# Performance work log

Measured on AMD Instinct MI355X. Metric: run time of the kernel, lower is better.

Reference implementation:

```python
import jax, jax.numpy as jnp
import numpy as np

H = 128  # hidden_size
EPS = 1e-5


def _lstm_scan(pre, Whh, h0, c0):
    # pre: [L, B, 4H] = x @ Wih^T + bias, precomputed outside the scan
    def step(carry, g_in):
        h, c = carry
        gates = g_in + h @ Whh.T  # [B, 4H], PyTorch gate order i,f,g,o
        i, f, g, o = jnp.split(gates, 4, axis=-1)
        c = jax.nn.sigmoid(f) * c + jax.nn.sigmoid(i) * jnp.tanh(g)
        h = jax.nn.sigmoid(o) * jnp.tanh(c)
        return (h, c), h
    (_, _), hs = jax.lax.scan(step, (h0, c0), pre)
    return hs  # [L, B, H]


def setup_inputs() -> dict:
    key = jax.random.key(0)
    ks = jax.random.split(key, 12)
    B, L, D = 128, 512, 256
    s = 0.05
    inp = {
        "x": jax.random.normal(ks[0], (B, L, D), jnp.float32),
        "W_proj": jax.random.normal(ks[1], (D, D), jnp.float32) * s,
        "b_proj": jnp.zeros((D,), jnp.float32),
        "Wih_f": jax.random.normal(ks[2], (4 * H, D), jnp.float32) * s,
        "Whh_f": jax.random.normal(ks[3], (4 * H, H), jnp.float32) * s,
        "b_f": jnp.concatenate([jnp.zeros(H), jnp.ones(H), jnp.zeros(2 * H)]).astype(jnp.float32),
        "Wih_b": jax.random.normal(ks[4], (4 * H, D), jnp.float32) * s,
        "Whh_b": jax.random.normal(ks[5], (4 * H, H), jnp.float32) * s,
        "b_b": jnp.concatenate([jnp.zeros(H), jnp.ones(H), jnp.zeros(2 * H)]).astype(jnp.float32),
        "gamma": jnp.ones((2 * H,), jnp.float32),
        "beta": jnp.zeros((2 * H,), jnp.float32),
    }
    return inp


def reference(x, W_proj, b_proj, Wih_f, Whh_f, b_f, Wih_b, Whh_b, b_b, gamma, beta):
    B, L, D = x.shape
    # input projection
    xp = x @ W_proj.T + b_proj  # [B, L, D]
    xt = jnp.transpose(xp, (1, 0, 2))  # time-major [L, B, D]

    h0 = jnp.zeros((B, H), x.dtype)
    c0 = jnp.zeros((B, H), x.dtype)

    # precompute input contributions to gates (big batched GEMM)
    pre_f = jnp.einsum('lbd,gd->lbg', xt, Wih_f) + b_f  # [L, B, 4H]
    pre_b = jnp.einsum('lbd,gd->lbg', xt[::-1], Wih_b) + b_b

    hs_f = _lstm_scan(pre_f, Whh_f, h0, c0)           # [L, B, H]
    hs_b = _lstm_scan(pre_b, Whh_b, h0, c0)[::-1]     # reverse back to forward time

    out = jnp.concatenate([hs_f, hs_b], axis=-1)       # [L, B, 2H]
    out = jnp.transpose(out, (1, 0, 2))                # [B, L, 2H]

    # LayerNorm over last dim (eval mode; dropout is identity)
    mu = out.mean(axis=-1, keepdims=True)
    var = out.var(axis=-1, keepdims=True)
    out = (out - mu) * jax.lax.rsqrt(var + EPS) * gamma + beta
    return out
```

## Files before the change

kernel.cpp:

```cpp
#include <hip/hip_runtime.h>

#define NB 128
#define NL 512
#define ND 256
#define NG 1024

typedef __attribute__((ext_vector_type(8))) short bfv8;
typedef __attribute__((ext_vector_type(4))) float f32x4;

#define LOG2E 1.4426950408889634f
#define NSCALE (-1.4426950408889634f)
#define GSCALE (2.8853900817779268f)

__device__ __forceinline__ unsigned short f2bf(float f) {
    unsigned u = __float_as_uint(f);
    u += 0x7fffu + ((u >> 16) & 1u);
    return (unsigned short)(u >> 16);
}
__device__ __forceinline__ float bf2f(unsigned short u) {
    return __uint_as_float(((unsigned)u) << 16);
}

__global__ __launch_bounds__(256) void convert_kernel(const float* __restrict__ x,
                                                      unsigned short* __restrict__ xbt) {
    size_t t = (size_t)blockIdx.x * 256 + threadIdx.x;
    size_t e = t * 4;
    int d = (int)(e & 255u);
    int l = (int)((e >> 8) & 511u);
    int b = (int)(e >> 17);
    float4 v = *(const float4*)(x + e);
    ushort4 o;
    o.x = f2bf(v.x); o.y = f2bf(v.y); o.z = f2bf(v.z); o.w = f2bf(v.w);
    *(ushort4*)(xbt + ((size_t)(l * NB + b)) * ND + d) = o;
}

__global__ __launch_bounds__(256) void fold_kernel(const float* __restrict__ Wproj,
                                                   const float* __restrict__ bproj,
                                                   const float* __restrict__ Wih_f,
                                                   const float* __restrict__ b_f,
                                                   const float* __restrict__ Wih_b,
                                                   const float* __restrict__ b_b,
                                                   unsigned short* __restrict__ weff,
                                                   float* __restrict__ beff) {
    int g = blockIdx.x;
    int k = threadIdx.x;
    int dirg = g >> 9;
    int rem  = g & 511;
    int hidg = rem >> 2;
    int gate = rem & 3;
    int srcrow = gate * 128 + hidg;
    float scale = (gate == 2) ? GSCALE : NSCALE;
    const float* Wih = dirg ? (Wih_b + (size_t)srcrow * ND) : (Wih_f + (size_t)srcrow * ND);
    float acc = 0.f;
    for (int d = 0; d < ND; ++d)
        acc += Wih[d] * Wproj[(size_t)d * ND + k];
    weff[(size_t)g * ND + k] = f2bf(acc * scale);
    if (k == 0) {
        float ab = dirg ? b_b[srcrow] : b_f[srcrow];
        for (int d = 0; d < ND; ++d) ab += Wih[d] * bproj[d];
        beff[g] = ab * scale;
    }
}

__global__ __launch_bounds__(256, 2) void gemm_pre(const unsigned short* __restrict__ A,
                                                   const unsigned short* __restrict__ Bw,
                                                   const float* __restrict__ bias,
                                                   unsigned short* __restrict__ C) {
    __shared__ unsigned short As[128 * 32];
    __shared__ unsigned short Bs[128 * 32];
    const int tid = threadIdx.x;
    const int lane = tid & 63;
    const int wid = tid >> 6;
    const int m0 = blockIdx.y * 128;
    const int n0 = blockIdx.x * 128;
    const int wm = (wid >> 1) * 64;
    const int wn = (wid & 1) * 64;

    f32x4 acc[4][4] = {};

    const int row0 = tid >> 2;
    const int row1 = row0 + 64;
    const int co = (tid & 3) * 8;
    const int sw = (((tid & 3) << 4) ^ ((row0 & 3) << 4)) >> 1;

    bfv8 ra0 = *(const bfv8*)(A + (size_t)(m0 + row0) * ND + co);
    bfv8 ra1 = *(const bfv8*)(A + (size_t)(m0 + row1) * ND + co);
    bfv8 rb0 = *(const bfv8*)(Bw + (size_t)(n0 + row0) * ND + co);
    bfv8 rb1 = *(const bfv8*)(Bw + (size_t)(n0 + row1) * ND + co);

    for (int it = 0; it < 8; ++it) {
        __syncthreads();
        *(bfv8*)(As + row0 * 32 + sw) = ra0;
        *(bfv8*)(As + row1 * 32 + sw) = ra1;
        *(bfv8*)(Bs + row0 * 32 + sw) = rb0;
        *(bfv8*)(Bs + row1 * 32 + sw) = rb1;
        const int k1 = ((it + 1) & 7) * 32;
        ra0 = *(const bfv8*)(A + (size_t)(m0 + row0) * ND + k1 + co);
        ra1 = *(const bfv8*)(A + (size_t)(m0 + row1) * ND + k1 + co);
        rb0 = *(const bfv8*)(Bw + (size_t)(n0 + row0) * ND + k1 + co);
        rb1 = *(const bfv8*)(Bw + (size_t)(n0 + row1) * ND + k1 + co);
        __syncthreads();

        const int r = lane & 15;
        const int kq = lane >> 4;
        bfv8 af[4], bfr[4];
        #pragma unroll
        for (int m = 0; m < 4; ++m) {
            int rw = wm + m * 16 + r;
            af[m] = *(const bfv8*)(As + rw * 32 + (((kq << 4) ^ ((rw & 3) << 4)) >> 1));
        }
        #pragma unroll
        for (int n = 0; n < 4; ++n) {
            int rw = wn + n * 16 + r;
            bfr[n] = *(const bfv8*)(Bs + rw * 32 + (((kq << 4) ^ ((rw & 3) << 4)) >> 1));
        }
        #pragma unroll
        for (int m = 0; m < 4; ++m)
            #pragma unroll
            for (int n = 0; n < 4; ++n)
                acc[m][n] = __builtin_amdgcn_mfma_f32_16x16x32_bf16(af[m], bfr[n], acc[m][n], 0, 0, 0);
    }

    const int r = lane & 15;
    const int rq = lane >> 4;
    #pragma unroll
    for (int n = 0; n < 4; ++n) {
        int col = n0 + wn + n * 16 + r;
        float bv = bias[col];
        #pragma unroll
        for (int m = 0; m < 4; ++m) {
            #pragma unroll
            for (int v = 0; v < 4; ++v) {
                int rowg = m0 + wm + m * 16 + rq * 4 + v;
                C[(size_t)rowg * NG + col] = f2bf(acc[m][n][v] + bv);
            }
        }
    }
}

struct ScanSM {
    unsigned short h[2][136];
    char pin[81700];
};

#define MFMA16(a, b, c) __builtin_amdgcn_mfma_f32_16x16x32_bf16((a), (b), (c), 0, 0, 0)

#define STEP(S, CURB, NXTB)                                                    \
  {                                                                            \
    int rr = (S) + 2; if (rr > 511) rr = 511;                \
    int tts = dirs ? (511 - rr) : rr;                                          \
    const unsigned short* rowp = pdb + (size_t)tts * (NB * NG);                \
    uint2 nx = *(const uint2*)(rowp + hid4);                \
    bfv8 ha0 = *(const bfv8*)&sm.h[CURB][q * 8];                               \
    bfv8 ha1 = *(const bfv8*)&sm.h[CURB][32 + q * 8];                          \
    bfv8 ha2 = *(const bfv8*)&sm.h[CURB][64 + q * 8];                          \
    bfv8 ha3 = *(const bfv8*)&sm.h[CURB][96 + q * 8];                          \
    f32x4 z = {0.f, 0.f, 0.f, 0.f};                                            \
    f32x4 iA = MFMA16(ha0, bfr[0][0], z);                                      \
    f32x4 fA = MFMA16(ha0, bfr[1][0], z);                                      \
    f32x4 gA = MFMA16(ha0, bfr[2][0], z);                                      \
    f32x4 oA = MFMA16(ha0, bfr[3][0], z);                                      \
    f32x4 iB = MFMA16(ha2, bfr[0][2], z);                                      \
    f32x4 fB = MFMA16(ha2, bfr[1][2], z);                                      \
    f32x4 gB = MFMA16(ha2, bfr[2][2], z);                                      \
    f32x4 oB = MFMA16(ha2, bfr[3][2], z);                                      \
    iA = MFMA16(ha1, bfr[0][1], iA); fA = MFMA16(ha1, bfr[1][1], fA);          \
    gA = MFMA16(ha1, bfr[2][1], gA); oA = MFMA16(ha1, bfr[3][1], oA);          \
    iB = MFMA16(ha3, bfr[0][3], iB); fB = MFMA16(ha3, bfr[1][3], fB);          \
    gB = MFMA16(ha3, bfr[2][3], gB); oB = MFMA16(ha3, bfr[3][3], oB);          \
    int tt = dirs ? (511 - (S)) : (S);                                         \
    {                                                                          \
        float pi = __uint_as_float(pP0.x << 16);                               \
        float pf = __uint_as_float(pP0.x & 0xffff0000u);                       \
        float pg = __uint_as_float(pP0.y << 16);                               \
        float po = __uint_as_float(pP0.y & 0xffff0000u);                       \
                 \
        float ia = __builtin_amdgcn_rcpf(1.f + __builtin_amdgcn_exp2f(iA[0] + iB[0] + pi)); \
        float fa = __builtin_amdgcn_rcpf(1.f + __builtin_amdgcn_exp2f(fA[0] + fB[0] + pf)); \
        float rg = __builtin_amdgcn_rcpf(1.f + __builtin_amdgcn_exp2f(gA[0] + gB[0] + pg)); \
        float oa = __builtin_amdgcn_rcpf(1.f + __builtin_amdgcn_exp2f(oA[0] + oB[0] + po)); \
        float ga = fmaf(-2.f, rg, 1.f);                                        \
        c0 = fmaf(fa, c0, ia * ga);                                            \
        float rc = __builtin_amdgcn_rcpf(1.f + __builtin_amdgcn_exp2f(c0 * GSCALE)); \
        float th = fmaf(-2.f, rc, 1.f);                                        \
        unsigned short us = f2bf(oa * th);                                     \
        if (q == 0) {                                                          \
            sm.h[NXTB][hid] = us;                                              \
            hsrow[(size_t)tt * 256 + hid] = us;                                \
        }                                                                      \
    }                                                                          \
    pP0 = pP1; pP1 = nx;                                                       \
    __builtin_amdgcn_sched_barrier(0);                                         \
    asm volatile("s_waitcnt lgkmcnt(0)");                                      \
    __builtin_amdgcn_s_barrier();                                              \
    __builtin_amdgcn_sched_barrier(0);                                         \
  }

__global__ void __launch_bounds__(512)
scan_kernel(const unsigned short* __restrict__ pre,
            const float* __restrict__ Whh_f,
            const float* __restrict__ Whh_b,
            unsigned short* __restrict__ hs) {
    const int b    = blockIdx.x;
    const int dirs = blockIdx.y;
    const int tid  = threadIdx.x;
    const int w    = tid >> 6;
    const int lane = tid & 63;
    const int r    = lane & 15;
    const int q    = lane >> 4;
    const int hid  = 16 * w + r;
    const int hid4 = hid * 4;

    __shared__ ScanSM sm;

    const float* __restrict__ Wd = dirs ? Whh_b : Whh_f;
    bfv8 bfr[4][4];
    #pragma unroll
    for (int g = 0; g < 4; ++g) {
        const float wscale = (g == 2) ? GSCALE : NSCALE;
        #pragma unroll
        for (int kk = 0; kk < 4; ++kk) {
            const float* src = Wd + (size_t)(g * 128 + hid) * 128 + kk * 32 + q * 8;
            float4 lo = *(const float4*)(src);
            float4 hi = *(const float4*)(src + 4);
            bfv8 v;
            v[0] = (short)f2bf(lo.x * wscale); v[1] = (short)f2bf(lo.y * wscale);
            v[2] = (short)f2bf(lo.z * wscale); v[3] = (short)f2bf(lo.w * wscale);
            v[4] = (short)f2bf(hi.x * wscale); v[5] = (short)f2bf(hi.y * wscale);
            v[6] = (short)f2bf(hi.z * wscale); v[7] = (short)f2bf(hi.w * wscale);
            bfr[g][kk] = v;
        }
    }

    if (q == 0) sm.h[0][hid] = 0;

    float c0 = 0.f;

    const unsigned short* pdb = pre + (size_t)b * NG + dirs * 512;
    unsigned short* hsrow = hs + (size_t)b * NL * 256 + dirs * 128;

    int t0 = dirs ? 511 : 0;
    int t1 = dirs ? 510 : 1;
    uint2 pP0 = *(const uint2*)(pdb + (size_t)t0 * (NB * NG) + hid4);
    uint2 pP1 = *(const uint2*)(pdb + (size_t)t1 * (NB * NG) + hid4);
    __syncthreads();

    for (int s = 0; s < 512; s += 2) {
        STEP(s, 0, 1)
        STEP(s + 1, 1, 0)
    }
}

__global__ __launch_bounds__(256) void ln_kernel(const unsigned short* __restrict__ hs,
                                                 float* __restrict__ out,
                                                 const float* __restrict__ gamma,
                                                 const float* __restrict__ beta) {
    int row = blockIdx.x * 4 + (threadIdx.x >> 6);
    int lane = threadIdx.x & 63;
    const ushort4 hv = ((const ushort4*)(hs + (size_t)row * 256))[lane];
    float a = bf2f(hv.x), bb = bf2f(hv.y), c = bf2f(hv.z), d = bf2f(hv.w);
    float s = (a + bb) + (c + d);
    float s2 = (a * a + bb * bb) + (c * c + d * d);
    #pragma unroll
    for (int o = 32; o > 0; o >>= 1) {
        s += __shfl_xor(s, o);
        s2 += __shfl_xor(s2, o);
    }
    float mu = s * (1.f / 256.f);
    float var = s2 * (1.f / 256.f) - mu * mu;
    float rs = rsqrtf(var + 1e-5f);
    float4 gv = ((const float4*)gamma)[lane];
    float4 bv = ((const float4*)beta)[lane];
    float4 rr;
    rr.x = (a - mu) * rs * gv.x + bv.x;
    rr.y = (bb - mu) * rs * gv.y + bv.y;
    rr.z = (c - mu) * rs * gv.z + bv.z;
    rr.w = (d - mu) * rs * gv.w + bv.w;
    ((float4*)(out + (size_t)row * 256))[lane] = rr;
}

extern "C" void kernel_launch(void* const* d_in, const int* in_sizes, int n_in,
                              void* d_out, int out_size, void* d_ws, size_t ws_size,
                              hipStream_t stream) {
    (void)in_sizes; (void)n_in; (void)out_size; (void)ws_size;
    const float* x     = (const float*)d_in[0];
    const float* Wproj = (const float*)d_in[1];
    const float* bproj = (const float*)d_in[2];
    const float* Wih_f = (const float*)d_in[3];
    const float* Whh_f = (const float*)d_in[4];
    const float* b_f   = (const float*)d_in[5];
    const float* Wih_b = (const float*)d_in[6];
    const float* Whh_b = (const float*)d_in[7];
    const float* b_b   = (const float*)d_in[8];
    const float* gamma = (const float*)d_in[9];
    const float* beta  = (const float*)d_in[10];
    float* out = (float*)d_out;

    char* ws = (char*)d_ws;
    unsigned short* pre  = (unsigned short*)ws;
    unsigned short* xbt  = (unsigned short*)(ws + 134217728);
    unsigned short* hs   = xbt;
    unsigned short* weff = (unsigned short*)(ws + 167772160);
    float*          beff = (float*)(ws + 168296448);

    convert_kernel<<<16384, 256, 0, stream>>>(x, xbt);
    fold_kernel<<<1024, 256, 0, stream>>>(Wproj, bproj, Wih_f, b_f, Wih_b, b_b, weff, beff);
    gemm_pre<<<dim3(8, 512), 256, 0, stream>>>(xbt, weff, beff, pre);
    scan_kernel<<<dim3(128, 2), 512, 0, stream>>>(pre, Whh_f, Whh_b, hs);
    ln_kernel<<<16384, 256, 0, stream>>>(hs, out, gamma, beta);
}
```

Baseline: 363.2 us.

## Use direct global-to-LDS loads in GEMM and single accumulator chain in LSTM step

The input-projection GEMM now uses global_load_lds to copy tiles straight into shared memory, with a source-side swizzle, in place of register-staged loads. The register prefetch of the next tile is dropped, so loads are issued and waited on within the same iteration. The recurrent step now chains all four K-chunks into one accumulator per gate instead of two partial accumulators summed afterwards. This saves adds and registers but lengthens the serial MFMA dependency chain on the latency-critical scan.

```diff
diff --git a/kernel.cpp b/kernel.cpp
--- a/kernel.cpp
+++ b/kernel.cpp
@@ -7,6 +7,9 @@
 
 typedef __attribute__((ext_vector_type(8))) short bfv8;
 typedef __attribute__((ext_vector_type(4))) float f32x4;
+
+typedef __attribute__((address_space(1))) const unsigned int glo_u32;
+typedef __attribute__((address_space(3))) unsigned int lds_u32;
 
 #define LOG2E 1.4426950408889634f
 #define NSCALE (-1.4426950408889634f)
@@ -78,27 +81,24 @@
 
     f32x4 acc[4][4] = {};
 
-    const int row0 = tid >> 2;
-    const int row1 = row0 + 64;
-    const int co = (tid & 3) * 8;
-    const int sw = (((tid & 3) << 4) ^ ((row0 & 3) << 4)) >> 1;
-
-    bfv8 ra0 = *(const bfv8*)(A + (size_t)(m0 + row0) * ND + co);
-    bfv8 ra1 = *(const bfv8*)(A + (size_t)(m0 + row1) * ND + co);
-    bfv8 rb0 = *(const bfv8*)(Bw + (size_t)(n0 + row0) * ND + co);
-    bfv8 rb1 = *(const bfv8*)(Bw + (size_t)(n0 + row1) * ND + co);
+    const int srow = tid >> 2;
+    const int csrc = (lane & 3) ^ (srow & 3);
+    unsigned short* a_l0 = As + wid * 512;
+    unsigned short* a_l1 = As + 2048 + wid * 512;
+    unsigned short* b_l0 = Bs + wid * 512;
+    unsigned short* b_l1 = Bs + 2048 + wid * 512;
 
     for (int it = 0; it < 8; ++it) {
         __syncthreads();
-        *(bfv8*)(As + row0 * 32 + sw) = ra0;
-        *(bfv8*)(As + row1 * 32 + sw) = ra1;
-        *(bfv8*)(Bs + row0 * 32 + sw) = rb0;
-        *(bfv8*)(Bs + row1 * 32 + sw) = rb1;
-        const int k1 = ((it + 1) & 7) * 32;
-        ra0 = *(const bfv8*)(A + (size_t)(m0 + row0) * ND + k1 + co);
-        ra1 = *(const bfv8*)(A + (size_t)(m0 + row1) * ND + k1 + co);
-        rb0 = *(const bfv8*)(Bw + (size_t)(n0 + row0) * ND + k1 + co);
-        rb1 = *(const bfv8*)(Bw + (size_t)(n0 + row1) * ND + k1 + co);
+        const int kb = it * 32;
+        const unsigned short* ga0 = A  + (size_t)(m0 + srow) * ND + kb + csrc * 8;
+        const unsigned short* ga1 = A  + (size_t)(m0 + srow + 64) * ND + kb + csrc * 8;
+        const unsigned short* gb0 = Bw + (size_t)(n0 + srow) * ND + kb + csrc * 8;
+        const unsigned short* gb1 = Bw + (size_t)(n0 + srow + 64) * ND + kb + csrc * 8;
+        __builtin_amdgcn_global_load_lds((glo_u32*)ga0, (lds_u32*)a_l0, 16, 0, 0);
+        __builtin_amdgcn_global_load_lds((glo_u32*)ga1, (lds_u32*)a_l1, 16, 0, 0);
+        __builtin_amdgcn_global_load_lds((glo_u32*)gb0, (lds_u32*)b_l0, 16, 0, 0);
+        __builtin_amdgcn_global_load_lds((glo_u32*)gb1, (lds_u32*)b_l1, 16, 0, 0);
         __syncthreads();
 
         const int r = lane & 15;
@@ -107,12 +107,12 @@
         #pragma unroll
         for (int m = 0; m < 4; ++m) {
             int rw = wm + m * 16 + r;
-            af[m] = *(const bfv8*)(As + rw * 32 + (((kq << 4) ^ ((rw & 3) << 4)) >> 1));
+            af[m] = *(const bfv8*)(As + rw * 32 + ((((kq << 4) ^ ((rw & 3) << 4))) >> 1));
         }
         #pragma unroll
         for (int n = 0; n < 4; ++n) {
             int rw = wn + n * 16 + r;
-            bfr[n] = *(const bfv8*)(Bs + rw * 32 + (((kq << 4) ^ ((rw & 3) << 4)) >> 1));
+            bfr[n] = *(const bfv8*)(Bs + rw * 32 + ((((kq << 4) ^ ((rw & 3) << 4))) >> 1));
         }
         #pragma unroll
         for (int m = 0; m < 4; ++m)
@@ -156,18 +156,16 @@
     bfv8 ha2 = *(const bfv8*)&sm.h[CURB][64 + q * 8];                          \
     bfv8 ha3 = *(const bfv8*)&sm.h[CURB][96 + q * 8];                          \
     f32x4 z = {0.f, 0.f, 0.f, 0.f};                                            \
-    f32x4 iA = MFMA16(ha0, bfr[0][0], z);                                      \
-    f32x4 fA = MFMA16(ha0, bfr[1][0], z);                                      \
-    f32x4 gA = MFMA16(ha0, bfr[2][0], z);                                      \
-    f32x4 oA = MFMA16(ha0, bfr[3][0], z);                                      \
-    f32x4 iB = MFMA16(ha2, bfr[0][2], z);                                      \
-    f32x4 fB = MFMA16(ha2, bfr[1][2], z);                                      \
-    f32x4 gB = MFMA16(ha2, bfr[2][2], z);                                      \
-    f32x4 oB = MFMA16(ha2, bfr[3][2], z);                                      \
-    iA = MFMA16(ha1, bfr[0][1], iA); fA = MFMA16(ha1, bfr[1][1], fA);          \
-    gA = MFMA16(ha1, bfr[2][1], gA); oA = MFMA16(ha1, bfr[3][1], oA);          \
-    iB = MFMA16(ha3, bfr[0][3], iB); fB = MFMA16(ha3, bfr[1][3], fB);          \
-    gB = MFMA16(ha3, bfr[2][3], gB); oB = MFMA16(ha3, bfr[3][3], oB);          \
+    f32x4 acci = MFMA16(ha0, bfr[0][0], z);                                    \
+    f32x4 accf = MFMA16(ha0, bfr[1][0], z);                                    \
+    f32x4 accg = MFMA16(ha0, bfr[2][0], z);                                    \
+    f32x4 acco = MFMA16(ha0, bfr[3][0], z);                                    \
+    acci = MFMA16(ha1, bfr[0][1], acci); accf = MFMA16(ha1, bfr[1][1], accf);  \
+    accg = MFMA16(ha1, bfr[2][1], accg); acco = MFMA16(ha1, bfr[3][1], acco);  \
+    acci = MFMA16(ha2, bfr[0][2], acci); accf = MFMA16(ha2, bfr[1][2], accf);  \
+    accg = MFMA16(ha2, bfr[2][2], accg); acco = MFMA16(ha2, bfr[3][2], acco);  \
+    acci = MFMA16(ha3, bfr[0][3], acci); accf = MFMA16(ha3, bfr[1][3], accf);  \
+    accg = MFMA16(ha3, bfr[2][3], accg); acco = MFMA16(ha3, bfr[3][3], acco);  \
     int tt = dirs ? (511 - (S)) : (S);                                         \
     {                                                                          \
         float pi = __uint_as_float(pP0.x << 16);                               \
@@ -175,10 +173,10 @@
         float pg = __uint_as_float(pP0.y << 16);                               \
         float po = __uint_as_float(pP0.y & 0xffff0000u);                       \
                  \
-        float ia = __builtin_amdgcn_rcpf(1.f + __builtin_amdgcn_exp2f(iA[0] + iB[0] + pi)); \
-        float fa = __builtin_amdgcn_rcpf(1.f + __builtin_amdgcn_exp2f(fA[0] + fB[0] + pf)); \
-        float rg = __builtin_amdgcn_rcpf(1.f + __builtin_amdgcn_exp2f(gA[0] + gB[0] + pg)); \
-        float oa = __builtin_amdgcn_rcpf(1.f + __builtin_amdgcn_exp2f(oA[0] + oB[0] + po)); \
+        float ia = __builtin_amdgcn_rcpf(1.f + __builtin_amdgcn_exp2f(acci[0] + pi)); \
+        float fa = __builtin_amdgcn_rcpf(1.f + __builtin_amdgcn_exp2f(accf[0] + pf)); \
+        float rg = __builtin_amdgcn_rcpf(1.f + __builtin_amdgcn_exp2f(accg[0] + pg)); \
+        float oa = __builtin_amdgcn_rcpf(1.f + __builtin_amdgcn_exp2f(acco[0] + po)); \
         float ga = fmaf(-2.f, rg, 1.f);                                        \
         c0 = fmaf(fa, c0, ia * ga);                                            \
         float rc = __builtin_amdgcn_rcpf(1.f + __builtin_amdgcn_exp2f(c0 * GSCALE)); \
```

Result: no change. 363.1 us (-0.0%).
